# Kernel optimization log

Measured on AMD Instinct MI355X. Metric: run time of the kernel, lower is better.

The kernel has to match this reference:

```python
import jax, jax.numpy as jnp
import numpy as np

N_NODES = 100000
N_EDGES = 1600000
IN_CH = 128
HID_CH = 128


def setup_inputs() -> dict:
    key = jax.random.key(0)
    ks = jax.random.split(key, 12)
    s = 1.0 / np.sqrt(IN_CH)
    sh = 1.0 / np.sqrt(HID_CH)
    return {
        "x": jax.random.normal(ks[0], (N_NODES, IN_CH), dtype=jnp.float32),
        "edge_index": jax.random.randint(ks[1], (2, N_EDGES), 0, N_NODES, dtype=jnp.int32),
        # SAGEConv1: lin_l (applied to aggregated neighbors, has bias), lin_r (root)
        "W1_l": jax.random.uniform(ks[2], (IN_CH, HID_CH), jnp.float32, -s, s),
        "b1": jax.random.uniform(ks[3], (HID_CH,), jnp.float32, -s, s),
        "W1_r": jax.random.uniform(ks[4], (IN_CH, HID_CH), jnp.float32, -s, s),
        # SAGEConv2
        "W2_l": jax.random.uniform(ks[5], (HID_CH, HID_CH), jnp.float32, -sh, sh),
        "b2": jax.random.uniform(ks[6], (HID_CH,), jnp.float32, -sh, sh),
        "W2_r": jax.random.uniform(ks[7], (HID_CH, HID_CH), jnp.float32, -sh, sh),
        # decoder Linear(hidden, in)
        "Wd": jax.random.uniform(ks[8], (HID_CH, IN_CH), jnp.float32, -sh, sh),
        "bd": jax.random.uniform(ks[9], (IN_CH,), jnp.float32, -sh, sh),
        "alpha": jnp.float32(0.5),
    }


def _sage_conv(h, src, dst, n_nodes, W_l, b, W_r):
    # PyG SAGEConv (mean aggr): out = lin_l(mean_{j in N(i)} x_j) + lin_r(x_i)
    msg = h[src]  # [E, C] gather from source nodes
    agg = jax.ops.segment_sum(msg, dst, num_segments=n_nodes)  # [N, C]
    cnt = jax.ops.segment_sum(jnp.ones((src.shape[0],), h.dtype), dst,
                              num_segments=n_nodes)  # [N]
    mean = agg / jnp.maximum(cnt, 1.0)[:, None]
    return mean @ W_l + b + h @ W_r


def reference(x, edge_index, W1_l, b1, W1_r, W2_l, b2, W2_r, Wd, bd, alpha):
    n_nodes = x.shape[0]
    src, dst = edge_index[0], edge_index[1]
    h = jax.nn.relu(_sage_conv(x, src, dst, n_nodes, W1_l, b1, W1_r))
    # dropout p=0.2 is identity in eval mode
    h = jax.nn.relu(_sage_conv(h, src, dst, n_nodes, W2_l, b2, W2_r))
    x_updated = h @ Wd + bd
    return alpha * x_updated + (1.0 - alpha) * x
```

## Files before the change

kernel.cpp:

```cpp
#include <hip/hip_runtime.h>
#include <cstddef>
#include <cstdint>

#define CH 128
#define NBKT 196
#define ABLK 320
#define BKT_NODES 512

typedef __attribute__((ext_vector_type(8))) short short8;
typedef __attribute__((ext_vector_type(4))) float f32x4;

__device__ __forceinline__ unsigned short f2bf(float f) {
  unsigned u = __float_as_uint(f);
  u += 0x7FFF + ((u >> 16) & 1);
  return (unsigned short)(u >> 16);
}
__device__ __forceinline__ float bf2f(unsigned int h) {
  return __uint_as_float(h << 16);
}
__device__ __forceinline__ void gld16(const void* g, void* l) {
  __builtin_amdgcn_global_load_lds((const __attribute__((address_space(1))) unsigned int*)g,
                                   (__attribute__((address_space(3))) unsigned int*)l, 16, 0, 0);
}

__global__ void k_cvt(const float4* __restrict__ in, uint4* __restrict__ out, int n8) {
  int i = blockIdx.x * 256 + threadIdx.x;
  if (i < n8) {
    float4 a = in[i * 2], b = in[i * 2 + 1];
    uint4 o;
    o.x = (unsigned)f2bf(a.x) | ((unsigned)f2bf(a.y) << 16);
    o.y = (unsigned)f2bf(a.z) | ((unsigned)f2bf(a.w) << 16);
    o.z = (unsigned)f2bf(b.x) | ((unsigned)f2bf(b.y) << 16);
    o.w = (unsigned)f2bf(b.z) | ((unsigned)f2bf(b.w) << 16);
    out[i] = o;
  }
}

__global__ void k_wt(const float* __restrict__ w0, const float* __restrict__ w1,
                     const float* __restrict__ w2, const float* __restrict__ w3,
                     const float* __restrict__ w4, unsigned short* __restrict__ dst) {
  const float* srcs[5] = {w0, w1, w2, w3, w4};
  const float* w = srcs[blockIdx.x];
  unsigned short* d = dst + (size_t)blockIdx.x * CH * CH;
  for (int idx = threadIdx.x; idx < CH * CH; idx += 256) {
    int k = idx >> 7, nn = idx & 127;
    d[nn * CH + k] = f2bf(w[idx]);
  }
}

__global__ void k_bhist(const int* __restrict__ dst, int* __restrict__ cnt, int E, int chunk) {
  __shared__ int c[NBKT];
  for (int i = threadIdx.x; i < NBKT; i += 256) c[i] = 0;
  __syncthreads();
  int s = blockIdx.x * chunk;
  int e = min(s + chunk, E);
  for (int i = s + threadIdx.x; i < e; i += 256)
    atomicAdd(&c[dst[i] >> 9], 1);
  __syncthreads();
  for (int i = threadIdx.x; i < NBKT; i += 256)
    cnt[i * ABLK + blockIdx.x] = c[i];
}

__global__ void k_bin(const int* __restrict__ src, const int* __restrict__ dst,
                      const int* __restrict__ ofs, unsigned int* __restrict__ binned,
                      int E, int chunk) {
  __shared__ int cur[NBKT];
  for (int i = threadIdx.x; i < NBKT; i += 256) cur[i] = ofs[i * ABLK + blockIdx.x];
  __syncthreads();
  int s = blockIdx.x * chunk;
  int e = min(s + chunk, E);
  for (int i = s + threadIdx.x; i < e; i += 256) {
    int d = dst[i];
    int b = d >> 9;
    int pos = atomicAdd(&cur[b], 1);
    binned[pos] = (unsigned)src[i] | ((unsigned)(d & 511) << 17);
  }
}

__global__ void k_deg(const unsigned int* __restrict__ binned, const int* __restrict__ ofs,
                      int* __restrict__ deg, int N) {
  __shared__ int c[BKT_NODES];
  int b = blockIdx.x;
  for (int i = threadIdx.x; i < BKT_NODES; i += 256) c[i] = 0;
  __syncthreads();
  int s = ofs[b * ABLK];
  int e = ofs[(b + 1) * ABLK];
  for (int i = s + threadIdx.x; i < e; i += 256)
    atomicAdd(&c[binned[i] >> 17], 1);
  __syncthreads();
  int base = b * BKT_NODES;
  for (int i = threadIdx.x; i < BKT_NODES; i += 256)
    if (base + i < N) deg[base + i] = c[i];
}

__global__ void k_sort(const unsigned int* __restrict__ binned, const int* __restrict__ ofs,
                       const int* __restrict__ rowptr, int* __restrict__ sorted, int N) {
  __shared__ int cur[BKT_NODES];
  int b = blockIdx.x;
  int base = b * BKT_NODES;
  for (int i = threadIdx.x; i < BKT_NODES; i += 256)
    cur[i] = (base + i < N) ? rowptr[base + i] : 0;
  __syncthreads();
  int s = ofs[b * ABLK];
  int e = ofs[(b + 1) * ABLK];
  for (int i = s + threadIdx.x; i < e; i += 256) {
    unsigned w = binned[i];
    int dl = w >> 17;
    int pos = atomicAdd(&cur[dl], 1);
    sorted[pos] = w & 0x1FFFF;
  }
}

__global__ void k_scan1(const int* __restrict__ deg, int* __restrict__ rowptr,
                        int* __restrict__ bsums, int n) {
  __shared__ int sh[256];
  int tid = threadIdx.x;
  int base = blockIdx.x * 1024 + tid * 4;
  int v0 = (base + 0 < n) ? deg[base + 0] : 0;
  int v1 = (base + 1 < n) ? deg[base + 1] : 0;
  int v2 = (base + 2 < n) ? deg[base + 2] : 0;
  int v3 = (base + 3 < n) ? deg[base + 3] : 0;
  int tot = v0 + v1 + v2 + v3;
  sh[tid] = tot;
  __syncthreads();
  for (int off = 1; off < 256; off <<= 1) {
    int y = (tid >= off) ? sh[tid - off] : 0;
    __syncthreads();
    sh[tid] += y;
    __syncthreads();
  }
  int excl = sh[tid] - tot;
  if (base + 0 < n) rowptr[base + 0] = excl;
  if (base + 1 < n) rowptr[base + 1] = excl + v0;
  if (base + 2 < n) rowptr[base + 2] = excl + v0 + v1;
  if (base + 3 < n) rowptr[base + 3] = excl + v0 + v1 + v2;
  if (tid == 255) bsums[blockIdx.x] = sh[255];
}

__global__ void k_scan2(int* __restrict__ bsums, int g) {
  __shared__ int sh[1024];
  int tid = threadIdx.x;
  int v = (tid < g) ? bsums[tid] : 0;
  sh[tid] = v;
  __syncthreads();
  for (int off = 1; off < 1024; off <<= 1) {
    int y = (tid >= off) ? sh[tid - off] : 0;
    __syncthreads();
    sh[tid] += y;
    __syncthreads();
  }
  if (tid < g) bsums[tid] = sh[tid] - v;
}

__global__ void k_scan3(int* __restrict__ arr, const int* __restrict__ bsums, int n, int total) {
  int i = blockIdx.x * 256 + threadIdx.x;
  if (i < n) arr[i] += bsums[i >> 10];
  if (i == 0) arr[n] = total;
}

__global__ __launch_bounds__(256)
void k_agg(const unsigned int* __restrict__ in, unsigned int* __restrict__ out,
           const int* __restrict__ rowptr, const int* __restrict__ sorted_src,
           int n, int nwaves) {
  int wid = (blockIdx.x * 256 + threadIdx.x) >> 6;
  int lane = threadIdx.x & 63;

  for (int node = wid; node < n; node += nwaves) {
    int beg = rowptr[node], end = rowptr[node + 1];
    float ax = 0.f, ay = 0.f;
    int e = beg;
    for (; e + 8 <= end; e += 8) {
      unsigned int v[8];
#pragma unroll
      for (int j = 0; j < 8; j++)
        v[j] = in[((unsigned)sorted_src[e + j] << 6) + lane];
#pragma unroll
      for (int j = 0; j < 8; j++) {
        ax += bf2f(v[j] & 0xffff);
        ay += bf2f(v[j] >> 16);
      }
    }
    if (e < end) {
      unsigned int v[8];
#pragma unroll
      for (int j = 0; j < 8; j++) {
        int idx = (e + j < end) ? (e + j) : beg;
        v[j] = in[((unsigned)sorted_src[idx] << 6) + lane];
      }
#pragma unroll
      for (int j = 0; j < 8; j++) {
        float lo = (e + j < end) ? bf2f(v[j] & 0xffff) : 0.f;
        float hi = (e + j < end) ? bf2f(v[j] >> 16) : 0.f;
        ax += lo;
        ay += hi;
      }
    }
    int d = end - beg;
    float inv = (d > 0) ? (1.f / (float)d) : 0.f;
    out[((unsigned)node << 6) + lane] =
        (unsigned)f2bf(ax * inv) | ((unsigned)f2bf(ay * inv) << 16);
  }
}

__global__ __launch_bounds__(256, 2)
void k_sage(const unsigned short* __restrict__ Am, const unsigned short* __restrict__ Ax,
            const unsigned short* __restrict__ WTl, const unsigned short* __restrict__ WTr,
            const float* __restrict__ bias, unsigned short* __restrict__ out, int n) {
  __shared__ unsigned short sA[128 * 64];
  __shared__ unsigned short sB[128 * 64];
  int tid = threadIdx.x;
  int lane = tid & 63;
  int w = tid >> 6;
  int row0 = blockIdx.x * 128;
  int col_lo = lane & 15, quad = lane >> 4;

  f32x4 acc[2][8];
#pragma unroll
  for (int mt = 0; mt < 2; mt++)
#pragma unroll
    for (int nt = 0; nt < 8; nt++) acc[mt][nt] = (f32x4){0.f, 0.f, 0.f, 0.f};

  const unsigned short* As[4] = {Am, Am, Ax, Ax};
  const unsigned short* Bs[4] = {WTl, WTl, WTr, WTr};
  const int k0s[4] = {0, 64, 0, 64};

  for (int c = 0; c < 4; c++) {
    const unsigned short* Ap = As[c];
    const unsigned short* Bp = Bs[c];
    int k0 = k0s[c];
#pragma unroll
    for (int it = 0; it < 4; it++) {
      int flat = it * 256 + tid;
      int r = flat >> 3;
      int kof = (flat & 7) * 8;
      int gr = row0 + r;
      if (gr > n - 1) gr = n - 1;
      gld16(Ap + (size_t)gr * CH + k0 + kof, sA + flat * 8);
      gld16(Bp + (size_t)r * CH + k0 + kof, sB + flat * 8);
    }
    __syncthreads();

#pragma unroll
    for (int ks = 0; ks < 2; ks++) {
      short8 a0 = *(const short8*)&sA[(w * 32 + col_lo) * 64 + ks * 32 + quad * 8];
      short8 a1 = *(const short8*)&sA[(w * 32 + 16 + col_lo) * 64 + ks * 32 + quad * 8];
      short8 b[8];
#pragma unroll
      for (int nt = 0; nt < 8; nt++)
        b[nt] = *(const short8*)&sB[(nt * 16 + col_lo) * 64 + ks * 32 + quad * 8];
#pragma unroll
      for (int nt = 0; nt < 8; nt++) {
        acc[0][nt] = __builtin_amdgcn_mfma_f32_16x16x32_bf16(a0, b[nt], acc[0][nt], 0, 0, 0);
        acc[1][nt] = __builtin_amdgcn_mfma_f32_16x16x32_bf16(a1, b[nt], acc[1][nt], 0, 0, 0);
      }
    }
    __syncthreads();
  }

#pragma unroll
  for (int nt = 0; nt < 8; nt++) {
    float bb = bias[nt * 16 + col_lo];
#pragma unroll
    for (int mt = 0; mt < 2; mt++) {
#pragma unroll
      for (int r = 0; r < 4; r++) {
        int rr = row0 + w * 32 + mt * 16 + quad * 4 + r;
        if (rr < n) {
          float v = fmaxf(acc[mt][nt][r] + bb, 0.f);
          out[(size_t)rr * CH + nt * 16 + col_lo] = f2bf(v);
        }
      }
    }
  }
}

__global__ __launch_bounds__(256, 2)
void k_dec(const unsigned short* __restrict__ H, const unsigned short* __restrict__ WTd,
           const float* __restrict__ bd, const float* __restrict__ X,
           const float* __restrict__ alpha_p, float* __restrict__ out, int n) {
  __shared__ unsigned short sA[128 * 64];
  __shared__ unsigned short sB[128 * 64];
  int tid = threadIdx.x;
  int lane = tid & 63;
  int w = tid >> 6;
  int row0 = blockIdx.x * 128;
  int col_lo = lane & 15, quad = lane >> 4;

  f32x4 acc[2][8];
#pragma unroll
  for (int mt = 0; mt < 2; mt++)
#pragma unroll
    for (int nt = 0; nt < 8; nt++) acc[mt][nt] = (f32x4){0.f, 0.f, 0.f, 0.f};

  for (int c = 0; c < 2; c++) {
    int k0 = c * 64;
#pragma unroll
    for (int it = 0; it < 4; it++) {
      int flat = it * 256 + tid;
      int r = flat >> 3;
      int kof = (flat & 7) * 8;
      int gr = row0 + r;
      if (gr > n - 1) gr = n - 1;
      gld16(H + (size_t)gr * CH + k0 + kof, sA + flat * 8);
      gld16(WTd + (size_t)r * CH + k0 + kof, sB + flat * 8);
    }
    __syncthreads();

#pragma unroll
    for (int ks = 0; ks < 2; ks++) {
      short8 a0 = *(const short8*)&sA[(w * 32 + col_lo) * 64 + ks * 32 + quad * 8];
      short8 a1 = *(const short8*)&sA[(w * 32 + 16 + col_lo) * 64 + ks * 32 + quad * 8];
      short8 b[8];
#pragma unroll
      for (int nt = 0; nt < 8; nt++)
        b[nt] = *(const short8*)&sB[(nt * 16 + col_lo) * 64 + ks * 32 + quad * 8];
#pragma unroll
      for (int nt = 0; nt < 8; nt++) {
        acc[0][nt] = __builtin_amdgcn_mfma_f32_16x16x32_bf16(a0, b[nt], acc[0][nt], 0, 0, 0);
        acc[1][nt] = __builtin_amdgcn_mfma_f32_16x16x32_bf16(a1, b[nt], acc[1][nt], 0, 0, 0);
      }
    }
    __syncthreads();
  }

  float al = alpha_p[0];
  float be = 1.f - al;
#pragma unroll
  for (int nt = 0; nt < 8; nt++) {
    float bb = bd[nt * 16 + col_lo];
#pragma unroll
    for (int mt = 0; mt < 2; mt++) {
#pragma unroll
      for (int r = 0; r < 4; r++) {
        int rr = row0 + w * 32 + mt * 16 + quad * 4 + r;
        if (rr < n) {
          int cc = nt * 16 + col_lo;
          float xv = X[(size_t)rr * CH + cc];
          out[(size_t)rr * CH + cc] = al * (acc[mt][nt][r] + bb) + be * xv;
        }
      }
    }
  }
}


extern "C" void kernel_launch(void* const* d_in, const int* in_sizes, int n_in,
                              void* d_out, int out_size, void* d_ws, size_t ws_size,
                              hipStream_t stream) {
  const float* x   = (const float*)d_in[0];
  const int*   ei  = (const int*)d_in[1];
  const float* W1l = (const float*)d_in[2];
  const float* b1  = (const float*)d_in[3];
  const float* W1r = (const float*)d_in[4];
  const float* W2l = (const float*)d_in[5];
  const float* b2  = (const float*)d_in[6];
  const float* W2r = (const float*)d_in[7];
  const float* Wd  = (const float*)d_in[8];
  const float* bd  = (const float*)d_in[9];
  const float* alp = (const float*)d_in[10];

  int N = in_sizes[0] / CH;
  int E = in_sizes[1] / 2;
  const int* src = ei;
  const int* dst = ei + E;

  char* ws = (char*)d_ws;
  size_t off = 0;
  auto alloc = [&](size_t bytes) -> char* {
    off = (off + 511) & ~size_t(511);
    char* p = ws + off;
    off += bytes;
    return p;
  };
  int*   deg    = (int*)alloc((size_t)N * 4);
  int*   rowptr = (int*)alloc((size_t)(N + 1) * 4);
  int*   ofs    = (int*)alloc((size_t)(NBKT * ABLK + 1) * 4);
  int*   bsums  = (int*)alloc(4096);
  int*   sorted = (int*)alloc((size_t)E * 4);
  unsigned short* xb = (unsigned short*)alloc((size_t)N * CH * 2);
  unsigned short* h  = (unsigned short*)alloc((size_t)N * CH * 2);
  unsigned short* WT = (unsigned short*)alloc((size_t)5 * CH * CH * 2);
  unsigned short* mean = (unsigned short*)d_out;
  unsigned int* binned = (unsigned int*)((char*)d_out + (size_t)N * CH * 2);

  int chunk = (E + ABLK - 1) / ABLK;
  int nA = NBKT * ABLK;
  int GA = (nA + 1023) / 1024;
  int GN = (N + 1023) / 1024;

  k_cvt<<<(N * CH / 8 + 255) / 256, 256, 0, stream>>>((const float4*)x, (uint4*)xb, N * CH / 8);
  k_wt<<<5, 256, 0, stream>>>(W1l, W1r, W2l, W2r, Wd, WT);

  k_bhist<<<ABLK, 256, 0, stream>>>(dst, ofs, E, chunk);
  k_scan1<<<GA, 256, 0, stream>>>(ofs, ofs, bsums, nA);
  k_scan2<<<1, 1024, 0, stream>>>(bsums, GA);
  k_scan3<<<(nA + 255) / 256, 256, 0, stream>>>(ofs, bsums, nA, E);
  k_bin<<<ABLK, 256, 0, stream>>>(src, dst, ofs, binned, E, chunk);
  k_deg<<<NBKT, 256, 0, stream>>>(binned, ofs, deg, N);
  k_scan1<<<GN, 256, 0, stream>>>(deg, rowptr, bsums, N);
  k_scan2<<<1, 1024, 0, stream>>>(bsums, GN);
  k_scan3<<<(N + 255) / 256, 256, 0, stream>>>(rowptr, bsums, N, E);
  k_sort<<<NBKT, 256, 0, stream>>>(binned, ofs, rowptr, sorted, N);

  int gAggBlocks = 2048;
  int nWaves = gAggBlocks * 4;
  int gGemm = (N + 127) / 128;
  unsigned short* WT1l = WT + 0 * CH * CH;
  unsigned short* WT1r = WT + 1 * CH * CH;
  unsigned short* WT2l = WT + 2 * CH * CH;
  unsigned short* WT2r = WT + 3 * CH * CH;
  unsigned short* WTd  = WT + 4 * CH * CH;

  k_agg<<<gAggBlocks, 256, 0, stream>>>((const unsigned int*)xb, (unsigned int*)mean,
                                        rowptr, sorted, N, nWaves);
  k_sage<<<gGemm, 256, 0, stream>>>(mean, xb, WT1l, WT1r, b1, h, N);
  k_agg<<<gAggBlocks, 256, 0, stream>>>((const unsigned int*)h, (unsigned int*)mean,
                                        rowptr, sorted, N, nWaves);
  k_sage<<<gGemm, 256, 0, stream>>>(mean, h, WT2l, WT2r, b2, h, N);
  k_dec<<<gGemm, 256, 0, stream>>>(h, WTd, bd, x, alp, (float*)d_out, N);
}
```

Before: 428.7 us.

## Fuse degree count, scan and sort into one bucket kernel; widen aggregation loads

Measured after the change: 421.3 us. Within noise of the previous version (-1.7%).

```diff
diff --git a/kernel.cpp b/kernel.cpp
--- a/kernel.cpp
+++ b/kernel.cpp
@@ -15,8 +15,11 @@
   u += 0x7FFF + ((u >> 16) & 1);
   return (unsigned short)(u >> 16);
 }
-__device__ __forceinline__ float bf2f(unsigned int h) {
-  return __uint_as_float(h << 16);
+__device__ __forceinline__ float bf_lo(unsigned int u) {
+  return __uint_as_float(u << 16);
+}
+__device__ __forceinline__ float bf_hi(unsigned int u) {
+  return __uint_as_float(u & 0xffff0000u);
 }
 __device__ __forceinline__ void gld16(const void* g, void* l) {
   __builtin_amdgcn_global_load_lds((const __attribute__((address_space(1))) unsigned int*)g,
@@ -77,38 +80,43 @@
   }
 }
 
-__global__ void k_deg(const unsigned int* __restrict__ binned, const int* __restrict__ ofs,
-                      int* __restrict__ deg, int N) {
+__global__ __launch_bounds__(256)
+void k_bucket(const unsigned int* __restrict__ binned, const int* __restrict__ ofs,
+              int* __restrict__ rowptr, int* __restrict__ sorted, int N, int E, int nbkt) {
   __shared__ int c[BKT_NODES];
-  int b = blockIdx.x;
-  for (int i = threadIdx.x; i < BKT_NODES; i += 256) c[i] = 0;
-  __syncthreads();
+  __shared__ int tsum[256];
+  __shared__ int cur[BKT_NODES];
+  int b = blockIdx.x, t = threadIdx.x;
   int s = ofs[b * ABLK];
   int e = ofs[(b + 1) * ABLK];
-  for (int i = s + threadIdx.x; i < e; i += 256)
+  c[t] = 0; c[t + 256] = 0;
+  __syncthreads();
+  for (int i = s + t; i < e; i += 256)
     atomicAdd(&c[binned[i] >> 17], 1);
   __syncthreads();
+  int v0 = c[2 * t], v1 = c[2 * t + 1];
+  int tot = v0 + v1;
+  tsum[t] = tot;
+  __syncthreads();
+  for (int o = 1; o < 256; o <<= 1) {
+    int y = (t >= o) ? tsum[t - o] : 0;
+    __syncthreads();
+    tsum[t] += y;
+    __syncthreads();
+  }
+  int excl = tsum[t] - tot;
   int base = b * BKT_NODES;
-  for (int i = threadIdx.x; i < BKT_NODES; i += 256)
-    if (base + i < N) deg[base + i] = c[i];
-}
-
-__global__ void k_sort(const unsigned int* __restrict__ binned, const int* __restrict__ ofs,
-                       const int* __restrict__ rowptr, int* __restrict__ sorted, int N) {
-  __shared__ int cur[BKT_NODES];
-  int b = blockIdx.x;
-  int base = b * BKT_NODES;
-  for (int i = threadIdx.x; i < BKT_NODES; i += 256)
-    cur[i] = (base + i < N) ? rowptr[base + i] : 0;
-  __syncthreads();
-  int s = ofs[b * ABLK];
-  int e = ofs[(b + 1) * ABLK];
-  for (int i = s + threadIdx.x; i < e; i += 256) {
+  int r0 = s + excl, r1 = s + excl + v0;
+  if (base + 2 * t < N)     rowptr[base + 2 * t]     = r0;
+  if (base + 2 * t + 1 < N) rowptr[base + 2 * t + 1] = r1;
+  cur[2 * t] = r0; cur[2 * t + 1] = r1;
+  __syncthreads();
+  for (int i = s + t; i < e; i += 256) {
     unsigned w = binned[i];
-    int dl = w >> 17;
-    int pos = atomicAdd(&cur[dl], 1);
+    int pos = atomicAdd(&cur[w >> 17], 1);
     sorted[pos] = w & 0x1FFFF;
   }
+  if (b == nbkt - 1 && t == 0) rowptr[N] = E;
 }
 
 __global__ void k_scan1(const int* __restrict__ deg, int* __restrict__ rowptr,
@@ -159,46 +167,57 @@
 }
 
 __global__ __launch_bounds__(256)
-void k_agg(const unsigned int* __restrict__ in, unsigned int* __restrict__ out,
+void k_agg(const uint2* __restrict__ in2, uint2* __restrict__ out2,
            const int* __restrict__ rowptr, const int* __restrict__ sorted_src,
            int n, int nwaves) {
   int wid = (blockIdx.x * 256 + threadIdx.x) >> 6;
   int lane = threadIdx.x & 63;
+  int half = lane >> 5;
+  int sl = lane & 31;
 
   for (int node = wid; node < n; node += nwaves) {
     int beg = rowptr[node], end = rowptr[node + 1];
-    float ax = 0.f, ay = 0.f;
+    float a0 = 0.f, a1 = 0.f, a2 = 0.f, a3 = 0.f;
     int e = beg;
     for (; e + 8 <= end; e += 8) {
-      unsigned int v[8];
-#pragma unroll
-      for (int j = 0; j < 8; j++)
-        v[j] = in[((unsigned)sorted_src[e + j] << 6) + lane];
-#pragma unroll
-      for (int j = 0; j < 8; j++) {
-        ax += bf2f(v[j] & 0xffff);
-        ay += bf2f(v[j] >> 16);
+      uint2 v[4];
+#pragma unroll
+      for (int j = 0; j < 4; j++)
+        v[j] = in2[((unsigned)sorted_src[e + 2 * j + half] << 5) + sl];
+#pragma unroll
+      for (int j = 0; j < 4; j++) {
+        a0 += bf_lo(v[j].x); a1 += bf_hi(v[j].x);
+        a2 += bf_lo(v[j].y); a3 += bf_hi(v[j].y);
       }
     }
     if (e < end) {
-      unsigned int v[8];
-#pragma unroll
-      for (int j = 0; j < 8; j++) {
-        int idx = (e + j < end) ? (e + j) : beg;
-        v[j] = in[((unsigned)sorted_src[idx] << 6) + lane];
-      }
-#pragma unroll
-      for (int j = 0; j < 8; j++) {
-        float lo = (e + j < end) ? bf2f(v[j] & 0xffff) : 0.f;
-        float hi = (e + j < end) ? bf2f(v[j] >> 16) : 0.f;
-        ax += lo;
-        ay += hi;
-      }
-    }
+      uint2 v[4];
+#pragma unroll
+      for (int j = 0; j < 4; j++) {
+        int k = e + 2 * j + half;
+        int idx = (k < end) ? k : beg;
+        uint2 tv = in2[((unsigned)sorted_src[idx] << 5) + sl];
+        if (k >= end) { tv.x = 0u; tv.y = 0u; }
+        v[j] = tv;
+      }
+#pragma unroll
+      for (int j = 0; j < 4; j++) {
+        a0 += bf_lo(v[j].x); a1 += bf_hi(v[j].x);
+        a2 += bf_lo(v[j].y); a3 += bf_hi(v[j].y);
+      }
+    }
+    a0 += __shfl(a0, lane ^ 32);
+    a1 += __shfl(a1, lane ^ 32);
+    a2 += __shfl(a2, lane ^ 32);
+    a3 += __shfl(a3, lane ^ 32);
     int d = end - beg;
     float inv = (d > 0) ? (1.f / (float)d) : 0.f;
-    out[((unsigned)node << 6) + lane] =
-        (unsigned)f2bf(ax * inv) | ((unsigned)f2bf(ay * inv) << 16);
+    if (half == 0) {
+      uint2 o;
+      o.x = (unsigned)f2bf(a0 * inv) | ((unsigned)f2bf(a1 * inv) << 16);
+      o.y = (unsigned)f2bf(a2 * inv) | ((unsigned)f2bf(a3 * inv) << 16);
+      out2[((unsigned)node << 5) + sl] = o;
+    }
   }
 }
 
@@ -372,7 +391,6 @@
     off += bytes;
     return p;
   };
-  int*   deg    = (int*)alloc((size_t)N * 4);
   int*   rowptr = (int*)alloc((size_t)(N + 1) * 4);
   int*   ofs    = (int*)alloc((size_t)(NBKT * ABLK + 1) * 4);
   int*   bsums  = (int*)alloc(4096);
@@ -386,7 +404,6 @@
   int chunk = (E + ABLK - 1) / ABLK;
   int nA = NBKT * ABLK;
   int GA = (nA + 1023) / 1024;
-  int GN = (N + 1023) / 1024;
 
   k_cvt<<<(N * CH / 8 + 255) / 256, 256, 0, stream>>>((const float4*)x, (uint4*)xb, N * CH / 8);
   k_wt<<<5, 256, 0, stream>>>(W1l, W1r, W2l, W2r, Wd, WT);
@@ -396,11 +413,7 @@
   k_scan2<<<1, 1024, 0, stream>>>(bsums, GA);
   k_scan3<<<(nA + 255) / 256, 256, 0, stream>>>(ofs, bsums, nA, E);
   k_bin<<<ABLK, 256, 0, stream>>>(src, dst, ofs, binned, E, chunk);
-  k_deg<<<NBKT, 256, 0, stream>>>(binned, ofs, deg, N);
-  k_scan1<<<GN, 256, 0, stream>>>(deg, rowptr, bsums, N);
-  k_scan2<<<1, 1024, 0, stream>>>(bsums, GN);
-  k_scan3<<<(N + 255) / 256, 256, 0, stream>>>(rowptr, bsums, N, E);
-  k_sort<<<NBKT, 256, 0, stream>>>(binned, ofs, rowptr, sorted, N);
+  k_bucket<<<NBKT, 256, 0, stream>>>(binned, ofs, rowptr, sorted, N, E, NBKT);
 
   int gAggBlocks = 2048;
   int nWaves = gAggBlocks * 4;
@@ -411,11 +424,9 @@
   unsigned short* WT2r = WT + 3 * CH * CH;
   unsigned short* WTd  = WT + 4 * CH * CH;
 
-  k_agg<<<gAggBlocks, 256, 0, stream>>>((const unsigned int*)xb, (unsigned int*)mean,
-                                        rowptr, sorted, N, nWaves);
+  k_agg<<<gAggBlocks, 256, 0, stream>>>((const uint2*)xb, (uint2*)mean, rowptr, sorted, N, nWaves);
   k_sage<<<gGemm, 256, 0, stream>>>(mean, xb, WT1l, WT1r, b1, h, N);
-  k_agg<<<gAggBlocks, 256, 0, stream>>>((const unsigned int*)h, (unsigned int*)mean,
-                                        rowptr, sorted, N, nWaves);
+  k_agg<<<gAggBlocks, 256, 0, stream>>>((const uint2*)h, (uint2*)mean, rowptr, sorted, N, nWaves);
   k_sage<<<gGemm, 256, 0, stream>>>(mean, h, WT2l, WT2r, b2, h, N);
   k_dec<<<gGemm, 256, 0, stream>>>(h, WTd, bd, x, alp, (float*)d_out, N);
 }
```
